# Optimization experiments

Measured on AMD Instinct MI355X. Metric: run time of the kernel, lower is better.

## Reference

```python
import jax, jax.numpy as jnp
import numpy as np

N = 50000
E = 500000
D = 128
L = 3
BN_EPS = 1e-5


def setup_inputs() -> dict:
    key = jax.random.key(0)
    ks = jax.random.split(key, 16)

    def xavier(k, shape):
        fan_in, fan_out = shape[-2], shape[-1]
        limit = float(np.sqrt(6.0 / (fan_in + fan_out)))
        return jax.random.uniform(k, shape, jnp.float32, -limit, limit)

    inp = {
        "x": jax.random.randint(ks[0], (N, 2), 0, 3),
        "edge_index": jax.random.randint(ks[1], (2, E), 0, N),
        "edge_attr": jax.random.randint(ks[2], (E, 2), 0, 3),
        # atom embeddings (xavier_uniform like torch init)
        "atom_emb0": xavier(ks[3], (120, D)),
        "atom_emb1": xavier(ks[4], (3, D)),
        # per-layer edge embeddings, stacked over layers
        "edge_emb0": xavier(ks[5], (L, 5, D)),
        "edge_emb1": xavier(ks[6], (L, 3, D)),
        # per-layer MLP: Linear(D, 2D) -> ReLU -> Linear(2D, D)
        "W1": xavier(ks[7], (L, D, 2 * D)),
        "b1": jnp.zeros((L, 2 * D), jnp.float32),
        "W2": xavier(ks[8], (L, 2 * D, D)),
        "b2": jnp.zeros((L, D), jnp.float32),
        # batchnorm affine params
        "gamma": jnp.ones((L, D), jnp.float32),
        "beta": jnp.zeros((L, D), jnp.float32),
    }
    return inp


def reference(x, edge_index, edge_attr, atom_emb0, atom_emb1,
              edge_emb0, edge_emb1, W1, b1, W2, b2, gamma, beta):
    n = x.shape[0]
    num_layer = W1.shape[0]

    # atom embedding: sum of per-attribute embeddings -> [N, D]
    h = atom_emb0[x[:, 0]] + atom_emb1[x[:, 1]]

    # add self loops: src/dst both get arange(N) appended
    loop = jnp.arange(n, dtype=edge_index.dtype)
    src = jnp.concatenate([edge_index[0], loop])  # [E+N]
    dst = jnp.concatenate([edge_index[1], loop])  # [E+N]
    # self-loop edge attr is [4, 0]
    ea0 = jnp.concatenate([edge_attr[:, 0], jnp.full((n,), 4, edge_attr.dtype)])
    ea1 = jnp.concatenate([edge_attr[:, 1], jnp.zeros((n,), edge_attr.dtype)])

    for l in range(num_layer):
        # edge embedding lookup + message = x_j + edge_attr, scatter-add to dst
        eemb = edge_emb0[l][ea0] + edge_emb1[l][ea1]          # [E+N, D]
        msg = h[src] + eemb                                   # gather + add
        aggr = jax.ops.segment_sum(msg, dst, num_segments=n)  # [N, D]
        # MLP update
        hid = jax.nn.relu(aggr @ W1[l] + b1[l])               # [N, 2D]
        out = hid @ W2[l] + b2[l]                             # [N, D]
        # BatchNorm1d (training mode: batch stats, biased variance)
        mean = jnp.mean(out, axis=0)
        var = jnp.mean(jnp.square(out - mean), axis=0)
        out = gamma[l] * (out - mean) * jax.lax.rsqrt(var + BN_EPS) + beta[l]
        # dropout with p=0 is identity; ReLU on all but last layer
        h = out if l == num_layer - 1 else jax.nn.relu(out)
    return h
```

## Files before the change

### kernel.cpp

```cpp
#include <hip/hip_runtime.h>

#define D 128
#define TWO_D 256
#define BN_EPS 1e-5f

typedef __attribute__((ext_vector_type(8))) short bf16x8;
typedef __attribute__((ext_vector_type(4))) float f32x4;

__device__ __forceinline__ float relu_f(float x) { return x > 0.f ? x : 0.f; }

__device__ __forceinline__ unsigned short f2bf(float f) {
    unsigned u = __builtin_bit_cast(unsigned, f);
    return (unsigned short)((u + 0x7FFFu + ((u >> 16) & 1u)) >> 16);
}
__device__ __forceinline__ float bf2f(unsigned s) {
    unsigned u = s << 16;
    return __builtin_bit_cast(float, u);
}
__device__ __forceinline__ unsigned pack2(float a, float b) {
    return (unsigned)f2bf(a) | ((unsigned)f2bf(b) << 16);
}

__global__ void atom_embed_kernel(const int* __restrict__ x,
                                  const float* __restrict__ emb0,
                                  const float* __restrict__ emb1,
                                  unsigned short* __restrict__ hbf, int n) {
    int idx = blockIdx.x * blockDim.x + threadIdx.x;
    if (idx >= n * 32) return;
    int node = idx >> 5;
    int d0 = (idx & 31) << 2;
    int i0 = x[node * 2 + 0];
    int i1 = x[node * 2 + 1];
    const float4 a = *reinterpret_cast<const float4*>(emb0 + (size_t)i0 * D + d0);
    const float4 b = *reinterpret_cast<const float4*>(emb1 + (size_t)i1 * D + d0);
    uint2 v;
    v.x = pack2(a.x + b.x, a.y + b.y);
    v.y = pack2(a.z + b.z, a.w + b.w);
    *reinterpret_cast<uint2*>(hbf + (size_t)node * D + d0) = v;
}

__global__ void hist_kernel(const int* __restrict__ ei, int* __restrict__ counts, int e_cnt) {
    int e = blockIdx.x * blockDim.x + threadIdx.x;
    if (e >= e_cnt) return;
    atomicAdd(counts + ei[e_cnt + e], 1);
}

__global__ __launch_bounds__(256) void bsum_kernel(const int* __restrict__ counts,
                                                   int* __restrict__ bsum, int n) {
    __shared__ int s[256];
    int t = threadIdx.x;
    int idx = blockIdx.x * 256 + t;
    s[t] = (idx < n) ? counts[idx] : 0;
    __syncthreads();
    for (int off = 128; off > 0; off >>= 1) {
        if (t < off) s[t] += s[t + off];
        __syncthreads();
    }
    if (t == 0) bsum[blockIdx.x] = s[0];
}

__global__ __launch_bounds__(256) void bscan_kernel(const int* __restrict__ bsum,
                                                    int* __restrict__ bpre,
                                                    int* __restrict__ row_ptr, int nb, int n) {
    __shared__ int s[256];
    int t = threadIdx.x;
    s[t] = (t < nb) ? bsum[t] : 0;
    __syncthreads();
    for (int off = 1; off < 256; off <<= 1) {
        int v = (t >= off) ? s[t - off] : 0;
        __syncthreads();
        s[t] += v;
        __syncthreads();
    }
    bpre[t] = (t == 0) ? 0 : s[t - 1];
    if (t == 255) row_ptr[n] = s[255];
}

__global__ __launch_bounds__(256) void scan_apply_kernel(const int* __restrict__ counts,
                                                         const int* __restrict__ bpre,
                                                         int* __restrict__ row_ptr,
                                                         int* __restrict__ cursor, int n) {
    __shared__ int s[256];
    int t = threadIdx.x;
    int idx = blockIdx.x * 256 + t;
    int c = (idx < n) ? counts[idx] : 0;
    s[t] = c;
    __syncthreads();
    for (int off = 1; off < 256; off <<= 1) {
        int v = (t >= off) ? s[t - off] : 0;
        __syncthreads();
        s[t] += v;
        __syncthreads();
    }
    if (idx < n) {
        int excl = bpre[blockIdx.x] + s[t] - c;
        row_ptr[idx] = excl;
        cursor[idx] = excl;
    }
}

__global__ void fill_kernel(const int* __restrict__ ei, const int* __restrict__ ea,
                            int* __restrict__ cursor, int* __restrict__ epack, int e_cnt) {
    int e = blockIdx.x * blockDim.x + threadIdx.x;
    if (e >= e_cnt) return;
    int dst = ei[e_cnt + e];
    int src = ei[e];
    int aidx = ea[e * 2 + 0] * 3 + ea[e * 2 + 1];
    int pos = atomicAdd(cursor + dst, 1);
    epack[pos] = (src & 0x1FFFF) | (aidx << 17);
}

__global__ void frag_prep_kernel(const float* __restrict__ W1,
                                 const float* __restrict__ W2,
                                 unsigned short* __restrict__ w1f,
                                 unsigned short* __restrict__ w2f, int Lnum) {
    int tid = blockIdx.x * blockDim.x + threadIdx.x;
    if (tid >= Lnum * 128 * 64) return;
    int l = tid / 8192;
    int rem = tid % 8192;
    int frag = rem / 64;
    int lane = rem % 64;
    int kg = lane >> 4, cl = lane & 15;
    if (frag < 64) {
        int kk = frag >> 4, tn = frag & 15;
        const float* src = W1 + (size_t)l * D * TWO_D;
        int k0 = kk * 32 + kg * 8, col = tn * 16 + cl;
        unsigned short* dst = w1f + (size_t)l * 32768 + ((size_t)frag * 64 + lane) * 8;
        #pragma unroll
        for (int j = 0; j < 8; ++j) dst[j] = f2bf(src[(size_t)(k0 + j) * TWO_D + col]);
    } else {
        int f2 = frag - 64;
        int kk = f2 >> 3, tn = f2 & 7;
        const float* src = W2 + (size_t)l * TWO_D * D;
        int k0 = kk * 32 + kg * 8, col = tn * 16 + cl;
        unsigned short* dst = w2f + (size_t)l * 32768 + ((size_t)f2 * 64 + lane) * 8;
        #pragma unroll
        for (int j = 0; j < 8; ++j) dst[j] = f2bf(src[(size_t)(k0 + j) * D + col]);
    }
}

template<int DO_BN>
__global__ __launch_bounds__(256) void gather_kernel(
    const unsigned short* __restrict__ hbf,
    const float* __restrict__ ee0_l, const float* __restrict__ ee1_l,
    const float* __restrict__ stats_prev,
    const float* __restrict__ gamma_p, const float* __restrict__ beta_p,
    float inv_n,
    const int* __restrict__ row_ptr, const int* __restrict__ epack,
    unsigned short* __restrict__ aggrbf, float* __restrict__ stats_cur, int n) {

    __shared__ float cee[16 * D];
    __shared__ float sbn[2 * D];
    const int t = threadIdx.x;
    if (blockIdx.x == 0) stats_cur[t] = 0.f;
    for (int i = t; i < 16 * D; i += 256) {
        int r = i >> 7, d = i & 127;
        cee[i] = (r < 15) ? ee0_l[(r / 3) * D + d] + ee1_l[(r % 3) * D + d]
                          : ee0_l[4 * D + d] + ee1_l[d];
    }
    if (DO_BN && t < 128) {
        float mean = stats_prev[t] * inv_n;
        float var  = stats_prev[128 + t] * inv_n - mean * mean;
        float sc = gamma_p[t] * rsqrtf(var + BN_EPS);
        sbn[t] = sc;
        sbn[128 + t] = beta_p[t] - mean * sc;
    }
    __syncthreads();

    int node = blockIdx.x * 8 + (t >> 5);
    if (node >= n) return;
    int d0 = (t & 31) << 2;

    float4 sc = make_float4(1.f, 1.f, 1.f, 1.f);
    float4 sh = make_float4(0.f, 0.f, 0.f, 0.f);
    if (DO_BN) {
        sc = *reinterpret_cast<const float4*>(sbn + d0);
        sh = *reinterpret_cast<const float4*>(sbn + 128 + d0);
    }

    const int jb = row_ptr[node];
    const int je = row_ptr[node + 1];

    float ax, ay, az, aw;
    {
        const float4 cs = *reinterpret_cast<const float4*>(cee + 15 * D + d0);
        uint2 hv = *reinterpret_cast<const uint2*>(hbf + (size_t)node * D + d0);
        if (DO_BN) {
            ax = relu_f(bf2f(hv.x & 0xffffu) * sc.x + sh.x) + cs.x;
            ay = relu_f(bf2f(hv.x >> 16)     * sc.y + sh.y) + cs.y;
            az = relu_f(bf2f(hv.y & 0xffffu) * sc.z + sh.z) + cs.z;
            aw = relu_f(bf2f(hv.y >> 16)     * sc.w + sh.w) + cs.w;
        } else {
            ax = bf2f(hv.x & 0xffffu) + cs.x;
            ay = bf2f(hv.x >> 16)     + cs.y;
            az = bf2f(hv.y & 0xffffu) + cs.z;
            aw = bf2f(hv.y >> 16)     + cs.w;
        }
    }

    unsigned long long c0 = 0ull;
    int cnt8 = 0;

#define ROWLD(p) (*reinterpret_cast<const uint2*>(hbf + (size_t)((p) & 0x1FFFF) * D + d0))
#define CNTUPD(p) do { int a_ = (p) >> 17; \
        unsigned long long bit_ = 1ull << ((a_ & 7) << 3); \
        c0 += (a_ < 8) ? bit_ : 0ull; cnt8 += (a_ >> 3); } while (0)
#define EACC(sv) do { \
        if (DO_BN) { \
            ax += relu_f(bf2f((sv).x & 0xffffu) * sc.x + sh.x); \
            ay += relu_f(bf2f((sv).x >> 16)     * sc.y + sh.y); \
            az += relu_f(bf2f((sv).y & 0xffffu) * sc.z + sh.z); \
            aw += relu_f(bf2f((sv).y >> 16)     * sc.w + sh.w); \
        } else { \
            ax += bf2f((sv).x & 0xffffu); ay += bf2f((sv).x >> 16); \
            az += bf2f((sv).y & 0xffffu); aw += bf2f((sv).y >> 16); \
        } } while (0)

    int j = jb;
    for (; j + 8 <= je; j += 8) {
        const int p0 = epack[j + 0], p1 = epack[j + 1], p2 = epack[j + 2], p3 = epack[j + 3];
        const int p4 = epack[j + 4], p5 = epack[j + 5], p6 = epack[j + 6], p7 = epack[j + 7];
        const uint2 s0 = ROWLD(p0), s1 = ROWLD(p1), s2 = ROWLD(p2), s3 = ROWLD(p3);
        const uint2 s4 = ROWLD(p4), s5 = ROWLD(p5), s6 = ROWLD(p6), s7 = ROWLD(p7);
        CNTUPD(p0); CNTUPD(p1); CNTUPD(p2); CNTUPD(p3);
        CNTUPD(p4); CNTUPD(p5); CNTUPD(p6); CNTUPD(p7);
        EACC(s0); EACC(s1); EACC(s2); EACC(s3);
        EACC(s4); EACC(s5); EACC(s6); EACC(s7);
    }
    for (; j < je; ++j) {
        const int p = epack[j];
        const uint2 sv = ROWLD(p);
        CNTUPD(p);
        EACC(sv);
    }

    #pragma unroll
    for (int a = 0; a < 8; ++a) {
        float fc = (float)((unsigned)(c0 >> (a * 8)) & 0xFFu);
        const float4 ev = *reinterpret_cast<const float4*>(cee + a * D + d0);
        ax += fc * ev.x; ay += fc * ev.y; az += fc * ev.z; aw += fc * ev.w;
    }
    {
        float fc = (float)cnt8;
        const float4 ev = *reinterpret_cast<const float4*>(cee + 8 * D + d0);
        ax += fc * ev.x; ay += fc * ev.y; az += fc * ev.z; aw += fc * ev.w;
    }

    uint2 o;
    o.x = pack2(ax, ay);
    o.y = pack2(az, aw);
    *reinterpret_cast<uint2*>(aggrbf + (size_t)node * D + d0) = o;
#undef ROWLD
#undef CNTUPD
#undef EACC
}

__global__ __launch_bounds__(256) void mlp_mfma_kernel(
    unsigned short* __restrict__ aggrbf,
    const bf16x8* __restrict__ w1f, const bf16x8* __restrict__ w2f,
    const float* __restrict__ b1l, const float* __restrict__ b2l,
    float* __restrict__ outf, float* __restrict__ stats, int n, int final_f32) {

    __shared__ unsigned short hid[32 * TWO_D];
    __shared__ float sred[256];

    const int wave = threadIdx.x >> 6;
    const int lane = threadIdx.x & 63;
    const int arow = lane & 15;
    const int kgrp = lane >> 4;

    bf16x8 W1[4][4];
    #pragma unroll
    for (int kk = 0; kk < 4; ++kk)
        #pragma unroll
        for (int t = 0; t < 4; ++t)
            W1[kk][t] = w1f[(kk * 16 + wave * 4 + t) * 64 + lane];
    bf16x8 W2[8][2];
    #pragma unroll
    for (int kk = 0; kk < 8; ++kk)
        #pragma unroll
        for (int t = 0; t < 2; ++t)
            W2[kk][t] = w2f[(kk * 8 + wave * 2 + t) * 64 + lane];

    float b1v[4], b2v[2];
    #pragma unroll
    for (int t = 0; t < 4; ++t) b1v[t] = b1l[wave * 64 + t * 16 + arow];
    #pragma unroll
    for (int t = 0; t < 2; ++t) b2v[t] = b2l[wave * 32 + t * 16 + arow];

    float ps[2] = {0.f, 0.f}, pq[2] = {0.f, 0.f};

    const int tiles = n >> 4;
    const int npair = (tiles + 1) >> 1;
    for (int p = blockIdx.x; p < npair; p += gridDim.x) {
        const int t0i = 2 * p, t1i = 2 * p + 1;
        const bool has1 = (t1i < tiles);
        const size_t r0 = (size_t)t0i * 16, r1 = (size_t)t1i * 16;

        bf16x8 a0[4], a1[4];
        #pragma unroll
        for (int kk = 0; kk < 4; ++kk)
            a0[kk] = *reinterpret_cast<const bf16x8*>(
                aggrbf + (r0 + arow) * D + kk * 32 + kgrp * 8);
        if (has1) {
            #pragma unroll
            for (int kk = 0; kk < 4; ++kk)
                a1[kk] = *reinterpret_cast<const bf16x8*>(
                    aggrbf + (r1 + arow) * D + kk * 32 + kgrp * 8);
        }

        f32x4 acc1[4];
        #pragma unroll
        for (int t = 0; t < 4; ++t) acc1[t] = (f32x4){0.f, 0.f, 0.f, 0.f};
        #pragma unroll
        for (int kk = 0; kk < 4; ++kk)
            #pragma unroll
            for (int t = 0; t < 4; ++t)
                acc1[t] = __builtin_amdgcn_mfma_f32_16x16x32_bf16(a0[kk], W1[kk][t], acc1[t], 0, 0, 0);

        __syncthreads();
        #pragma unroll
        for (int t = 0; t < 4; ++t) {
            const int cc = wave * 64 + t * 16 + arow;
            #pragma unroll
            for (int r = 0; r < 4; ++r) {
                const int rr = kgrp * 4 + r;
                hid[(rr * TWO_D + cc) ^ ((rr & 7) << 3)] = f2bf(relu_f(acc1[t][r] + b1v[t]));
            }
        }

        if (has1) {
            #pragma unroll
            for (int t = 0; t < 4; ++t) acc1[t] = (f32x4){0.f, 0.f, 0.f, 0.f};
            #pragma unroll
            for (int kk = 0; kk < 4; ++kk)
                #pragma unroll
                for (int t = 0; t < 4; ++t)
                    acc1[t] = __builtin_amdgcn_mfma_f32_16x16x32_bf16(a1[kk], W1[kk][t], acc1[t], 0, 0, 0);
            #pragma unroll
            for (int t = 0; t < 4; ++t) {
                const int cc = wave * 64 + t * 16 + arow;
                #pragma unroll
                for (int r = 0; r < 4; ++r) {
                    const int rr = 16 + kgrp * 4 + r;
                    hid[(rr * TWO_D + cc) ^ ((rr & 7) << 3)] = f2bf(relu_f(acc1[t][r] + b1v[t]));
                }
            }
        }
        __syncthreads();

        {
            f32x4 acc2[2];
            #pragma unroll
            for (int t = 0; t < 2; ++t) acc2[t] = (f32x4){0.f, 0.f, 0.f, 0.f};
            #pragma unroll
            for (int kk = 0; kk < 8; ++kk) {
                bf16x8 a2 = *reinterpret_cast<const bf16x8*>(
                    hid + ((arow * TWO_D + kk * 32 + kgrp * 8) ^ ((arow & 7) << 3)));
                #pragma unroll
                for (int t = 0; t < 2; ++t)
                    acc2[t] = __builtin_amdgcn_mfma_f32_16x16x32_bf16(a2, W2[kk][t], acc2[t], 0, 0, 0);
            }
            #pragma unroll
            for (int t = 0; t < 2; ++t) {
                const int col = wave * 32 + t * 16 + arow;
                #pragma unroll
                for (int r = 0; r < 4; ++r) {
                    float v = acc2[t][r] + b2v[t];
                    if (final_f32) outf[(r0 + kgrp * 4 + r) * D + col] = v;
                    else           aggrbf[(r0 + kgrp * 4 + r) * D + col] = f2bf(v);
                    ps[t] += v; pq[t] += v * v;
                }
            }
        }
        if (has1) {
            f32x4 acc2[2];
            #pragma unroll
            for (int t = 0; t < 2; ++t) acc2[t] = (f32x4){0.f, 0.f, 0.f, 0.f};
            #pragma unroll
            for (int kk = 0; kk < 8; ++kk) {
                bf16x8 a2 = *reinterpret_cast<const bf16x8*>(
                    hid + (((16 + arow) * TWO_D + kk * 32 + kgrp * 8) ^ ((arow & 7) << 3)));
                #pragma unroll
                for (int t = 0; t < 2; ++t)
                    acc2[t] = __builtin_amdgcn_mfma_f32_16x16x32_bf16(a2, W2[kk][t], acc2[t], 0, 0, 0);
            }
            #pragma unroll
            for (int t = 0; t < 2; ++t) {
                const int col = wave * 32 + t * 16 + arow;
                #pragma unroll
                for (int r = 0; r < 4; ++r) {
                    float v = acc2[t][r] + b2v[t];
                    if (final_f32) outf[(r1 + kgrp * 4 + r) * D + col] = v;
                    else           aggrbf[(r1 + kgrp * 4 + r) * D + col] = f2bf(v);
                    ps[t] += v; pq[t] += v * v;
                }
            }
        }
    }

    sred[threadIdx.x] = 0.f;
    __syncthreads();
    #pragma unroll
    for (int t = 0; t < 2; ++t) {
        const int col = wave * 32 + t * 16 + arow;
        atomicAdd(sred + col, ps[t]);
        atomicAdd(sred + 128 + col, pq[t]);
    }
    __syncthreads();
    unsafeAtomicAdd(stats + threadIdx.x, sred[threadIdx.x]);
}

__global__ void bn_apply_final_kernel(const float* __restrict__ out,
                                      const float* __restrict__ stats,
                                      const float* __restrict__ gamma_l,
                                      const float* __restrict__ beta_l,
                                      float inv_n,
                                      float* __restrict__ dst, int n) {
    __shared__ float sbn[2 * D];
    int t = threadIdx.x;
    if (t < 128) {
        float mean = stats[t] * inv_n;
        float var  = stats[128 + t] * inv_n - mean * mean;
        float sc = gamma_l[t] * rsqrtf(var + BN_EPS);
        sbn[t] = sc;
        sbn[128 + t] = beta_l[t] - mean * sc;
    }
    __syncthreads();
    int idx = blockIdx.x * blockDim.x + t;
    if (idx >= n * 32) return;
    int d0 = (idx & 31) << 2;
    float4 v  = *reinterpret_cast<const float4*>(out + (size_t)idx * 4);
    float4 sc = *reinterpret_cast<const float4*>(sbn + d0);
    float4 sh = *reinterpret_cast<const float4*>(sbn + 128 + d0);
    *reinterpret_cast<float4*>(dst + (size_t)idx * 4) =
        make_float4(v.x * sc.x + sh.x, v.y * sc.y + sh.y,
                    v.z * sc.z + sh.z, v.w * sc.w + sh.w);
}

extern "C" void kernel_launch(void* const* d_in, const int* in_sizes, int n_in,
                              void* d_out, int out_size, void* d_ws, size_t ws_size,
                              hipStream_t stream) {
    const int*   x     = (const int*)d_in[0];
    const int*   ei    = (const int*)d_in[1];
    const int*   ea    = (const int*)d_in[2];
    const float* aemb0 = (const float*)d_in[3];
    const float* aemb1 = (const float*)d_in[4];
    const float* eemb0 = (const float*)d_in[5];
    const float* eemb1 = (const float*)d_in[6];
    const float* W1    = (const float*)d_in[7];
    const float* b1    = (const float*)d_in[8];
    const float* W2    = (const float*)d_in[9];
    const float* b2    = (const float*)d_in[10];
    const float* gamma = (const float*)d_in[11];
    const float* beta  = (const float*)d_in[12];

    const int n = in_sizes[0] / 2;
    const int e = in_sizes[1] / 2;
    const int L = in_sizes[8] / TWO_D;
    const float inv_n = 1.0f / (float)n;

    char* ws = (char*)d_ws;
    float* outb = (float*)ws;                      ws += (size_t)n * D * 4;
    unsigned short* bufA = (unsigned short*)ws;    ws += (size_t)n * D * 2;
    unsigned short* bufB = (unsigned short*)ws;    ws += (size_t)n * D * 2;
    unsigned short* w1f = (unsigned short*)ws;     ws += (size_t)L * 32768 * 2;
    unsigned short* w2f = (unsigned short*)ws;     ws += (size_t)L * 32768 * 2;
    float* statsA = (float*)ws;                    ws += 256 * 4;
    float* statsB = (float*)ws;                    ws += 256 * 4;
    int* counts  = (int*)ws;                       ws += (size_t)n * 4;
    int* row_ptr = (int*)ws;                       ws += (size_t)(n + 1) * 4;
    int* cursor  = (int*)ws;                       ws += (size_t)n * 4;
    int* bsum    = (int*)ws;                       ws += 256 * 4;
    int* bpre    = (int*)ws;                       ws += 256 * 4;
    int* epack   = (int*)ws;

    const int edge_blocks = (e + 255) / 256;
    const int vec_blocks  = (n * 32 + 255) / 256;
    const int node_blocks = (n + 7) / 8;
    const int nb = (n + 255) / 256;

    hipMemsetAsync(counts, 0, (size_t)n * sizeof(int), stream);
    hist_kernel<<<edge_blocks, 256, 0, stream>>>(ei, counts, e);
    bsum_kernel<<<nb, 256, 0, stream>>>(counts, bsum, n);
    bscan_kernel<<<1, 256, 0, stream>>>(bsum, bpre, row_ptr, nb, n);
    scan_apply_kernel<<<nb, 256, 0, stream>>>(counts, bpre, row_ptr, cursor, n);
    fill_kernel<<<edge_blocks, 256, 0, stream>>>(ei, ea, cursor, epack, e);
    frag_prep_kernel<<<(L * 128 * 64 + 255) / 256, 256, 0, stream>>>(W1, W2, w1f, w2f, L);
    atom_embed_kernel<<<vec_blocks, 256, 0, stream>>>(x, aemb0, aemb1, bufA, n);

    for (int l = 0; l < L; ++l) {
        const float* ee0_l = eemb0 + (size_t)l * 5 * D;
        const float* ee1_l = eemb1 + (size_t)l * 3 * D;
        const float* b1l   = b1 + (size_t)l * TWO_D;
        const float* b2l   = b2 + (size_t)l * D;

        unsigned short* src = (l & 1) ? bufB : bufA;
        unsigned short* dst = (l & 1) ? bufA : bufB;
        float* stats_cur  = (l & 1) ? statsB : statsA;
        float* stats_prev = (l & 1) ? statsA : statsB;

        if (l == 0)
            gather_kernel<0><<<node_blocks, 256, 0, stream>>>(
                src, ee0_l, ee1_l, nullptr, nullptr, nullptr, inv_n,
                row_ptr, epack, dst, stats_cur, n);
        else
            gather_kernel<1><<<node_blocks, 256, 0, stream>>>(
                src, ee0_l, ee1_l, stats_prev,
                gamma + (size_t)(l - 1) * D, beta + (size_t)(l - 1) * D, inv_n,
                row_ptr, epack, dst, stats_cur, n);

        mlp_mfma_kernel<<<512, 256, 0, stream>>>(
            dst,
            (const bf16x8*)(w1f + (size_t)l * 32768),
            (const bf16x8*)(w2f + (size_t)l * 32768),
            b1l, b2l, outb, stats_cur, n, (l == L - 1) ? 1 : 0);
    }

    float* stats_last = ((L - 1) & 1) ? statsB : statsA;
    bn_apply_final_kernel<<<vec_blocks, 256, 0, stream>>>(
        outb, stats_last, gamma + (size_t)(L - 1) * D, beta + (size_t)(L - 1) * D,
        inv_n, (float*)d_out, n);
}
```

Baseline: 278.8 us.

## Pad CSR rows to multiples of 8 with 16-bit source ids and separate BN pass

The CSR build now pads each row to a multiple of eight entries, filling the padding with a zero node row, and stores source indices as 16-bit values. Edge-attribute counts are computed once per node in the histogram kernel rather than decoded per edge on every layer. The gather kernel loads eight indices at a time with one vector load and uses no tail loop. BatchNorm plus ReLU moves out of the gather's per-edge path into a separate bn_mid kernel that writes bf16 once per layer, which adds a full pass over an fp32 buffer each layer. The 16-bit indices rely on N fitting in 16 bits, and the padding adds gather reads of the zero row.

```diff
diff --git a/kernel.cpp b/kernel.cpp
--- a/kernel.cpp
+++ b/kernel.cpp
@@ -25,6 +25,8 @@
                                   const float* __restrict__ emb0,
                                   const float* __restrict__ emb1,
                                   unsigned short* __restrict__ hbf, int n) {
+    if (blockIdx.x == 0 && threadIdx.x < 64)
+        reinterpret_cast<unsigned*>(hbf + (size_t)n * D)[threadIdx.x] = 0u;
     int idx = blockIdx.x * blockDim.x + threadIdx.x;
     if (idx >= n * 32) return;
     int node = idx >> 5;
@@ -39,18 +41,25 @@
     *reinterpret_cast<uint2*>(hbf + (size_t)node * D + d0) = v;
 }
 
-__global__ void hist_kernel(const int* __restrict__ ei, int* __restrict__ counts, int e_cnt) {
+__global__ void hist_kernel(const int* __restrict__ ei, const int* __restrict__ ea,
+                            int* __restrict__ counts,
+                            unsigned long long* __restrict__ cnts, int e_cnt) {
     int e = blockIdx.x * blockDim.x + threadIdx.x;
     if (e >= e_cnt) return;
-    atomicAdd(counts + ei[e_cnt + e], 1);
-}
+    int dst = ei[e_cnt + e];
+    atomicAdd(counts + dst, 1);
+    int aidx = ea[e * 2 + 0] * 3 + ea[e * 2 + 1];
+    if (aidx < 8) atomicAdd(cnts + dst, 1ull << (aidx * 8));
+}
+
+__device__ __forceinline__ int pad8(int d) { return (d + 7) & ~7; }
 
 __global__ __launch_bounds__(256) void bsum_kernel(const int* __restrict__ counts,
                                                    int* __restrict__ bsum, int n) {
     __shared__ int s[256];
     int t = threadIdx.x;
     int idx = blockIdx.x * 256 + t;
-    s[t] = (idx < n) ? counts[idx] : 0;
+    s[t] = (idx < n) ? pad8(counts[idx]) : 0;
     __syncthreads();
     for (int off = 128; off > 0; off >>= 1) {
         if (t < off) s[t] += s[t + off];
@@ -61,7 +70,7 @@
 
 __global__ __launch_bounds__(256) void bscan_kernel(const int* __restrict__ bsum,
                                                     int* __restrict__ bpre,
-                                                    int* __restrict__ row_ptr, int nb, int n) {
+                                                    int* __restrict__ rpp, int nb, int n) {
     __shared__ int s[256];
     int t = threadIdx.x;
     s[t] = (t < nb) ? bsum[t] : 0;
@@ -73,17 +82,17 @@
         __syncthreads();
     }
     bpre[t] = (t == 0) ? 0 : s[t - 1];
-    if (t == 255) row_ptr[n] = s[255];
+    if (t == 255) rpp[n] = s[255];
 }
 
 __global__ __launch_bounds__(256) void scan_apply_kernel(const int* __restrict__ counts,
                                                          const int* __restrict__ bpre,
-                                                         int* __restrict__ row_ptr,
+                                                         int* __restrict__ rpp,
                                                          int* __restrict__ cursor, int n) {
     __shared__ int s[256];
     int t = threadIdx.x;
     int idx = blockIdx.x * 256 + t;
-    int c = (idx < n) ? counts[idx] : 0;
+    int c = (idx < n) ? pad8(counts[idx]) : 0;
     s[t] = c;
     __syncthreads();
     for (int off = 1; off < 256; off <<= 1) {
@@ -94,20 +103,31 @@
     }
     if (idx < n) {
         int excl = bpre[blockIdx.x] + s[t] - c;
-        row_ptr[idx] = excl;
+        rpp[idx] = excl;
         cursor[idx] = excl;
     }
 }
 
-__global__ void fill_kernel(const int* __restrict__ ei, const int* __restrict__ ea,
-                            int* __restrict__ cursor, int* __restrict__ epack, int e_cnt) {
+__global__ void fill_kernel(const int* __restrict__ ei,
+                            int* __restrict__ cursor,
+                            unsigned short* __restrict__ ep, int e_cnt) {
     int e = blockIdx.x * blockDim.x + threadIdx.x;
     if (e >= e_cnt) return;
     int dst = ei[e_cnt + e];
     int src = ei[e];
-    int aidx = ea[e * 2 + 0] * 3 + ea[e * 2 + 1];
     int pos = atomicAdd(cursor + dst, 1);
-    epack[pos] = (src & 0x1FFFF) | (aidx << 17);
+    ep[pos] = (unsigned short)src;
+}
+
+__global__ void pad_kernel(const int* __restrict__ cursor, const int* __restrict__ counts,
+                           const int* __restrict__ rpp,
+                           unsigned short* __restrict__ ep, int n) {
+    int i = blockIdx.x * blockDim.x + threadIdx.x;
+    if (i >= n) return;
+    int b = cursor[i];
+    int e = rpp[i] + pad8(counts[i]);
+    unsigned short zr = (unsigned short)n;
+    for (int j = b; j < e; ++j) ep[j] = zr;
 }
 
 __global__ void frag_prep_kernel(const float* __restrict__ W1,
@@ -139,127 +159,94 @@
     }
 }
 
-template<int DO_BN>
 __global__ __launch_bounds__(256) void gather_kernel(
     const unsigned short* __restrict__ hbf,
     const float* __restrict__ ee0_l, const float* __restrict__ ee1_l,
-    const float* __restrict__ stats_prev,
-    const float* __restrict__ gamma_p, const float* __restrict__ beta_p,
-    float inv_n,
-    const int* __restrict__ row_ptr, const int* __restrict__ epack,
-    unsigned short* __restrict__ aggrbf, float* __restrict__ stats_cur, int n) {
+    const int* __restrict__ rpp, const int* __restrict__ counts,
+    const unsigned long long* __restrict__ cnts,
+    const unsigned short* __restrict__ ep,
+    unsigned short* __restrict__ aggrbf, float* __restrict__ stats, int n) {
 
     __shared__ float cee[16 * D];
-    __shared__ float sbn[2 * D];
     const int t = threadIdx.x;
-    if (blockIdx.x == 0) stats_cur[t] = 0.f;
+    if (blockIdx.x == 0) stats[t] = 0.f;
     for (int i = t; i < 16 * D; i += 256) {
         int r = i >> 7, d = i & 127;
         cee[i] = (r < 15) ? ee0_l[(r / 3) * D + d] + ee1_l[(r % 3) * D + d]
                           : ee0_l[4 * D + d] + ee1_l[d];
     }
-    if (DO_BN && t < 128) {
-        float mean = stats_prev[t] * inv_n;
-        float var  = stats_prev[128 + t] * inv_n - mean * mean;
-        float sc = gamma_p[t] * rsqrtf(var + BN_EPS);
-        sbn[t] = sc;
-        sbn[128 + t] = beta_p[t] - mean * sc;
-    }
     __syncthreads();
 
     int node = blockIdx.x * 8 + (t >> 5);
     if (node >= n) return;
     int d0 = (t & 31) << 2;
 
-    float4 sc = make_float4(1.f, 1.f, 1.f, 1.f);
-    float4 sh = make_float4(0.f, 0.f, 0.f, 0.f);
-    if (DO_BN) {
-        sc = *reinterpret_cast<const float4*>(sbn + d0);
-        sh = *reinterpret_cast<const float4*>(sbn + 128 + d0);
-    }
-
-    const int jb = row_ptr[node];
-    const int je = row_ptr[node + 1];
+    const int jb = rpp[node];
+    const int deg = counts[node];
+    const unsigned long long c0 = cnts[node];
+    const int nch = pad8(deg) >> 3;
 
     float ax, ay, az, aw;
     {
         const float4 cs = *reinterpret_cast<const float4*>(cee + 15 * D + d0);
         uint2 hv = *reinterpret_cast<const uint2*>(hbf + (size_t)node * D + d0);
-        if (DO_BN) {
-            ax = relu_f(bf2f(hv.x & 0xffffu) * sc.x + sh.x) + cs.x;
-            ay = relu_f(bf2f(hv.x >> 16)     * sc.y + sh.y) + cs.y;
-            az = relu_f(bf2f(hv.y & 0xffffu) * sc.z + sh.z) + cs.z;
-            aw = relu_f(bf2f(hv.y >> 16)     * sc.w + sh.w) + cs.w;
-        } else {
-            ax = bf2f(hv.x & 0xffffu) + cs.x;
-            ay = bf2f(hv.x >> 16)     + cs.y;
-            az = bf2f(hv.y & 0xffffu) + cs.z;
-            aw = bf2f(hv.y >> 16)     + cs.w;
-        }
-    }
-
-    unsigned long long c0 = 0ull;
-    int cnt8 = 0;
-
-#define ROWLD(p) (*reinterpret_cast<const uint2*>(hbf + (size_t)((p) & 0x1FFFF) * D + d0))
-#define CNTUPD(p) do { int a_ = (p) >> 17; \
-        unsigned long long bit_ = 1ull << ((a_ & 7) << 3); \
-        c0 += (a_ < 8) ? bit_ : 0ull; cnt8 += (a_ >> 3); } while (0)
-#define EACC(sv) do { \
-        if (DO_BN) { \
-            ax += relu_f(bf2f((sv).x & 0xffffu) * sc.x + sh.x); \
-            ay += relu_f(bf2f((sv).x >> 16)     * sc.y + sh.y); \
-            az += relu_f(bf2f((sv).y & 0xffffu) * sc.z + sh.z); \
-            aw += relu_f(bf2f((sv).y >> 16)     * sc.w + sh.w); \
-        } else { \
-            ax += bf2f((sv).x & 0xffffu); ay += bf2f((sv).x >> 16); \
-            az += bf2f((sv).y & 0xffffu); aw += bf2f((sv).y >> 16); \
-        } } while (0)
-
-    int j = jb;
-    for (; j + 8 <= je; j += 8) {
-        const int p0 = epack[j + 0], p1 = epack[j + 1], p2 = epack[j + 2], p3 = epack[j + 3];
-        const int p4 = epack[j + 4], p5 = epack[j + 5], p6 = epack[j + 6], p7 = epack[j + 7];
-        const uint2 s0 = ROWLD(p0), s1 = ROWLD(p1), s2 = ROWLD(p2), s3 = ROWLD(p3);
-        const uint2 s4 = ROWLD(p4), s5 = ROWLD(p5), s6 = ROWLD(p6), s7 = ROWLD(p7);
-        CNTUPD(p0); CNTUPD(p1); CNTUPD(p2); CNTUPD(p3);
-        CNTUPD(p4); CNTUPD(p5); CNTUPD(p6); CNTUPD(p7);
-        EACC(s0); EACC(s1); EACC(s2); EACC(s3);
-        EACC(s4); EACC(s5); EACC(s6); EACC(s7);
-    }
-    for (; j < je; ++j) {
-        const int p = epack[j];
-        const uint2 sv = ROWLD(p);
-        CNTUPD(p);
-        EACC(sv);
-    }
-
+        ax = bf2f(hv.x & 0xffffu) + cs.x;
+        ay = bf2f(hv.x >> 16)     + cs.y;
+        az = bf2f(hv.y & 0xffffu) + cs.z;
+        aw = bf2f(hv.y >> 16)     + cs.w;
+    }
+
+    int csum = 0;
     #pragma unroll
     for (int a = 0; a < 8; ++a) {
-        float fc = (float)((unsigned)(c0 >> (a * 8)) & 0xFFu);
+        int fc = (int)((c0 >> (a * 8)) & 0xFFull);
+        csum += fc;
+        float f = (float)fc;
         const float4 ev = *reinterpret_cast<const float4*>(cee + a * D + d0);
-        ax += fc * ev.x; ay += fc * ev.y; az += fc * ev.z; aw += fc * ev.w;
+        ax += f * ev.x; ay += f * ev.y; az += f * ev.z; aw += f * ev.w;
     }
     {
-        float fc = (float)cnt8;
+        float f = (float)(deg - csum);
         const float4 ev = *reinterpret_cast<const float4*>(cee + 8 * D + d0);
-        ax += fc * ev.x; ay += fc * ev.y; az += fc * ev.z; aw += fc * ev.w;
-    }
+        ax += f * ev.x; ay += f * ev.y; az += f * ev.z; aw += f * ev.w;
+    }
+
+#define ROWLD(s) (*reinterpret_cast<const uint2*>(hbf + (size_t)(s) * D + d0))
+#define EACC(sv) do { \
+        ax += bf2f((sv).x & 0xffffu); ay += bf2f((sv).x >> 16); \
+        az += bf2f((sv).y & 0xffffu); aw += bf2f((sv).y >> 16); } while (0)
+#define PROC(iv) do { \
+        const uint2 s0 = ROWLD((iv).x & 0xFFFFu), s1 = ROWLD((iv).x >> 16); \
+        const uint2 s2 = ROWLD((iv).y & 0xFFFFu), s3 = ROWLD((iv).y >> 16); \
+        const uint2 s4 = ROWLD((iv).z & 0xFFFFu), s5 = ROWLD((iv).z >> 16); \
+        const uint2 s6 = ROWLD((iv).w & 0xFFFFu), s7 = ROWLD((iv).w >> 16); \
+        EACC(s0); EACC(s1); EACC(s2); EACC(s3); \
+        EACC(s4); EACC(s5); EACC(s6); EACC(s7); } while (0)
+
+    if (nch) {
+        uint4 iv = *reinterpret_cast<const uint4*>(ep + jb);
+        for (int c = 1; c < nch; ++c) {
+            uint4 nx = *reinterpret_cast<const uint4*>(ep + jb + 8 * c);
+            PROC(iv);
+            iv = nx;
+        }
+        PROC(iv);
+    }
+#undef ROWLD
+#undef EACC
+#undef PROC
 
     uint2 o;
     o.x = pack2(ax, ay);
     o.y = pack2(az, aw);
     *reinterpret_cast<uint2*>(aggrbf + (size_t)node * D + d0) = o;
-#undef ROWLD
-#undef CNTUPD
-#undef EACC
 }
 
 __global__ __launch_bounds__(256) void mlp_mfma_kernel(
-    unsigned short* __restrict__ aggrbf,
+    const unsigned short* __restrict__ aggrbf,
     const bf16x8* __restrict__ w1f, const bf16x8* __restrict__ w2f,
     const float* __restrict__ b1l, const float* __restrict__ b2l,
-    float* __restrict__ outf, float* __restrict__ stats, int n, int final_f32) {
+    float* __restrict__ outf, float* __restrict__ stats, int n) {
 
     __shared__ unsigned short hid[32 * TWO_D];
     __shared__ float sred[256];
@@ -328,7 +315,6 @@
                 hid[(rr * TWO_D + cc) ^ ((rr & 7) << 3)] = f2bf(relu_f(acc1[t][r] + b1v[t]));
             }
         }
-
         if (has1) {
             #pragma unroll
             for (int t = 0; t < 4; ++t) acc1[t] = (f32x4){0.f, 0.f, 0.f, 0.f};
@@ -367,8 +353,7 @@
                 #pragma unroll
                 for (int r = 0; r < 4; ++r) {
                     float v = acc2[t][r] + b2v[t];
-                    if (final_f32) outf[(r0 + kgrp * 4 + r) * D + col] = v;
-                    else           aggrbf[(r0 + kgrp * 4 + r) * D + col] = f2bf(v);
+                    outf[(r0 + kgrp * 4 + r) * D + col] = v;
                     ps[t] += v; pq[t] += v * v;
                 }
             }
@@ -391,8 +376,7 @@
                 #pragma unroll
                 for (int r = 0; r < 4; ++r) {
                     float v = acc2[t][r] + b2v[t];
-                    if (final_f32) outf[(r1 + kgrp * 4 + r) * D + col] = v;
-                    else           aggrbf[(r1 + kgrp * 4 + r) * D + col] = f2bf(v);
+                    outf[(r1 + kgrp * 4 + r) * D + col] = v;
                     ps[t] += v; pq[t] += v * v;
                 }
             }
@@ -409,6 +393,36 @@
     }
     __syncthreads();
     unsafeAtomicAdd(stats + threadIdx.x, sred[threadIdx.x]);
+}
+
+__global__ void bn_mid_kernel(const float* __restrict__ out,
+                              const float* __restrict__ stats,
+                              const float* __restrict__ gamma_l,
+                              const float* __restrict__ beta_l,
+                              float inv_n,
+                              unsigned short* __restrict__ dsth, int n) {
+    __shared__ float sbn[2 * D];
+    int t = threadIdx.x;
+    if (blockIdx.x == 0 && t >= 128 && t < 192)
+        reinterpret_cast<unsigned*>(dsth + (size_t)n * D)[t - 128] = 0u;
+    if (t < 128) {
+        float mean = stats[t] * inv_n;
+        float var  = stats[128 + t] * inv_n - mean * mean;
+        float sc = gamma_l[t] * rsqrtf(var + BN_EPS);
+        sbn[t] = sc;
+        sbn[128 + t] = beta_l[t] - mean * sc;
+    }
+    __syncthreads();
+    int idx = blockIdx.x * blockDim.x + t;
+    if (idx >= n * 32) return;
+    int d0 = (idx & 31) << 2;
+    float4 v  = *reinterpret_cast<const float4*>(out + (size_t)idx * 4);
+    float4 sc = *reinterpret_cast<const float4*>(sbn + d0);
+    float4 sh = *reinterpret_cast<const float4*>(sbn + 128 + d0);
+    uint2 o;
+    o.x = pack2(relu_f(v.x * sc.x + sh.x), relu_f(v.y * sc.y + sh.y));
+    o.y = pack2(relu_f(v.z * sc.z + sh.z), relu_f(v.w * sc.w + sh.w));
+    *reinterpret_cast<uint2*>(dsth + (size_t)idx * 4) = o;
 }
 
 __global__ void bn_apply_final_kernel(const float* __restrict__ out,
@@ -462,63 +476,58 @@
 
     char* ws = (char*)d_ws;
     float* outb = (float*)ws;                      ws += (size_t)n * D * 4;
-    unsigned short* bufA = (unsigned short*)ws;    ws += (size_t)n * D * 2;
-    unsigned short* bufB = (unsigned short*)ws;    ws += (size_t)n * D * 2;
+    unsigned short* buf0 = (unsigned short*)ws;    ws += (size_t)(n + 1) * D * 2;
+    unsigned short* buf1 = (unsigned short*)ws;    ws += (size_t)(n + 1) * D * 2;
+    unsigned short* bufC = (unsigned short*)ws;    ws += (size_t)n * D * 2;
     unsigned short* w1f = (unsigned short*)ws;     ws += (size_t)L * 32768 * 2;
     unsigned short* w2f = (unsigned short*)ws;     ws += (size_t)L * 32768 * 2;
-    float* statsA = (float*)ws;                    ws += 256 * 4;
-    float* statsB = (float*)ws;                    ws += 256 * 4;
+    float* stats = (float*)ws;                     ws += 256 * 4;
     int* counts  = (int*)ws;                       ws += (size_t)n * 4;
-    int* row_ptr = (int*)ws;                       ws += (size_t)(n + 1) * 4;
+    unsigned long long* cnts = (unsigned long long*)ws;  ws += (size_t)n * 8;
+    int* rpp     = (int*)ws;                       ws += (size_t)(n + 4) * 4;
     int* cursor  = (int*)ws;                       ws += (size_t)n * 4;
     int* bsum    = (int*)ws;                       ws += 256 * 4;
     int* bpre    = (int*)ws;                       ws += 256 * 4;
-    int* epack   = (int*)ws;
+    unsigned short* epack = (unsigned short*)ws;
 
     const int edge_blocks = (e + 255) / 256;
     const int vec_blocks  = (n * 32 + 255) / 256;
     const int node_blocks = (n + 7) / 8;
     const int nb = (n + 255) / 256;
 
-    hipMemsetAsync(counts, 0, (size_t)n * sizeof(int), stream);
-    hist_kernel<<<edge_blocks, 256, 0, stream>>>(ei, counts, e);
+    hipMemsetAsync(counts, 0, (size_t)n * 4 + (size_t)n * 8, stream);
+    hist_kernel<<<edge_blocks, 256, 0, stream>>>(ei, ea, counts, cnts, e);
     bsum_kernel<<<nb, 256, 0, stream>>>(counts, bsum, n);
-    bscan_kernel<<<1, 256, 0, stream>>>(bsum, bpre, row_ptr, nb, n);
-    scan_apply_kernel<<<nb, 256, 0, stream>>>(counts, bpre, row_ptr, cursor, n);
-    fill_kernel<<<edge_blocks, 256, 0, stream>>>(ei, ea, cursor, epack, e);
+    bscan_kernel<<<1, 256, 0, stream>>>(bsum, bpre, rpp, nb, n);
+    scan_apply_kernel<<<nb, 256, 0, stream>>>(counts, bpre, rpp, cursor, n);
+    fill_kernel<<<edge_blocks, 256, 0, stream>>>(ei, cursor, epack, e);
+    pad_kernel<<<nb, 256, 0, stream>>>(cursor, counts, rpp, epack, n);
     frag_prep_kernel<<<(L * 128 * 64 + 255) / 256, 256, 0, stream>>>(W1, W2, w1f, w2f, L);
-    atom_embed_kernel<<<vec_blocks, 256, 0, stream>>>(x, aemb0, aemb1, bufA, n);
+    atom_embed_kernel<<<vec_blocks, 256, 0, stream>>>(x, aemb0, aemb1, buf0, n);
 
     for (int l = 0; l < L; ++l) {
         const float* ee0_l = eemb0 + (size_t)l * 5 * D;
         const float* ee1_l = eemb1 + (size_t)l * 3 * D;
-        const float* b1l   = b1 + (size_t)l * TWO_D;
-        const float* b2l   = b2 + (size_t)l * D;
-
-        unsigned short* src = (l & 1) ? bufB : bufA;
-        unsigned short* dst = (l & 1) ? bufA : bufB;
-        float* stats_cur  = (l & 1) ? statsB : statsA;
-        float* stats_prev = (l & 1) ? statsA : statsB;
-
-        if (l == 0)
-            gather_kernel<0><<<node_blocks, 256, 0, stream>>>(
-                src, ee0_l, ee1_l, nullptr, nullptr, nullptr, inv_n,
-                row_ptr, epack, dst, stats_cur, n);
-        else
-            gather_kernel<1><<<node_blocks, 256, 0, stream>>>(
-                src, ee0_l, ee1_l, stats_prev,
-                gamma + (size_t)(l - 1) * D, beta + (size_t)(l - 1) * D, inv_n,
-                row_ptr, epack, dst, stats_cur, n);
-
+
+        unsigned short* hsrc = (l & 1) ? buf1 : buf0;
+
+        gather_kernel<<<node_blocks, 256, 0, stream>>>(
+            hsrc, ee0_l, ee1_l, rpp, counts, cnts, epack, bufC, stats, n);
         mlp_mfma_kernel<<<512, 256, 0, stream>>>(
-            dst,
+            bufC,
             (const bf16x8*)(w1f + (size_t)l * 32768),
             (const bf16x8*)(w2f + (size_t)l * 32768),
-            b1l, b2l, outb, stats_cur, n, (l == L - 1) ? 1 : 0);
-    }
-
-    float* stats_last = ((L - 1) & 1) ? statsB : statsA;
-    bn_apply_final_kernel<<<vec_blocks, 256, 0, stream>>>(
-        outb, stats_last, gamma + (size_t)(L - 1) * D, beta + (size_t)(L - 1) * D,
-        inv_n, (float*)d_out, n);
-}
+            b1 + (size_t)l * TWO_D, b2 + (size_t)l * D, outb, stats, n);
+
+        if (l < L - 1) {
+            unsigned short* hdst = (l & 1) ? buf0 : buf1;
+            bn_mid_kernel<<<vec_blocks, 256, 0, stream>>>(
+                outb, stats, gamma + (size_t)l * D, beta + (size_t)l * D,
+                inv_n, hdst, n);
+        } else {
+            bn_apply_final_kernel<<<vec_blocks, 256, 0, stream>>>(
+                outb, stats, gamma + (size_t)l * D, beta + (size_t)l * D,
+                inv_n, (float*)d_out, n);
+        }
+    }
+}
```

Measured after the change: 301.0 us. +8.0%, slower.

## Pad CSR rows to 8 with 16-bit source indices and precomputed attr counts

Applied to the files above, without the earlier changes.

Rebuilds the CSR so each node's edge list is padded to a multiple of 8 and stores source indices as 16-bit values in a new conversion pass. That pass also precomputes per-node edge-attribute counts. The gather kernel then loads 8 indices with a single 128-bit load, prefetches the next chunk, and skips per-edge attribute decoding. Padding slots point at a zero row appended to each feature buffer, and under batchnorm the ReLU of the shift is subtracted for them. Risk: 16-bit indices cannot address N=50000 plus the zero row beyond 65535, so this depends on N staying small; it also adds a setup kernel and extra workspace.

```diff
diff --git a/kernel.cpp b/kernel.cpp
--- a/kernel.cpp
+++ b/kernel.cpp
@@ -21,10 +21,17 @@
     return (unsigned)f2bf(a) | ((unsigned)f2bf(b) << 16);
 }
 
+__device__ __forceinline__ int pad8(int d) { return (d + 7) & ~7; }
+
 __global__ void atom_embed_kernel(const int* __restrict__ x,
                                   const float* __restrict__ emb0,
                                   const float* __restrict__ emb1,
-                                  unsigned short* __restrict__ hbf, int n) {
+                                  unsigned short* __restrict__ bufA,
+                                  unsigned short* __restrict__ bufB, int n) {
+    if (blockIdx.x == 0 && threadIdx.x < 64)
+        reinterpret_cast<unsigned*>(bufA + (size_t)n * D)[threadIdx.x] = 0u;
+    if (blockIdx.x == 1 && threadIdx.x < 64)
+        reinterpret_cast<unsigned*>(bufB + (size_t)n * D)[threadIdx.x] = 0u;
     int idx = blockIdx.x * blockDim.x + threadIdx.x;
     if (idx >= n * 32) return;
     int node = idx >> 5;
@@ -36,7 +43,7 @@
     uint2 v;
     v.x = pack2(a.x + b.x, a.y + b.y);
     v.y = pack2(a.z + b.z, a.w + b.w);
-    *reinterpret_cast<uint2*>(hbf + (size_t)node * D + d0) = v;
+    *reinterpret_cast<uint2*>(bufA + (size_t)node * D + d0) = v;
 }
 
 __global__ void hist_kernel(const int* __restrict__ ei, int* __restrict__ counts, int e_cnt) {
@@ -50,7 +57,7 @@
     __shared__ int s[256];
     int t = threadIdx.x;
     int idx = blockIdx.x * 256 + t;
-    s[t] = (idx < n) ? counts[idx] : 0;
+    s[t] = (idx < n) ? pad8(counts[idx]) : 0;
     __syncthreads();
     for (int off = 128; off > 0; off >>= 1) {
         if (t < off) s[t] += s[t + off];
@@ -61,7 +68,7 @@
 
 __global__ __launch_bounds__(256) void bscan_kernel(const int* __restrict__ bsum,
                                                     int* __restrict__ bpre,
-                                                    int* __restrict__ row_ptr, int nb, int n) {
+                                                    int* __restrict__ rpp, int nb, int n) {
     __shared__ int s[256];
     int t = threadIdx.x;
     s[t] = (t < nb) ? bsum[t] : 0;
@@ -73,17 +80,17 @@
         __syncthreads();
     }
     bpre[t] = (t == 0) ? 0 : s[t - 1];
-    if (t == 255) row_ptr[n] = s[255];
+    if (t == 255) rpp[n] = s[255];
 }
 
 __global__ __launch_bounds__(256) void scan_apply_kernel(const int* __restrict__ counts,
                                                          const int* __restrict__ bpre,
-                                                         int* __restrict__ row_ptr,
+                                                         int* __restrict__ rpp,
                                                          int* __restrict__ cursor, int n) {
     __shared__ int s[256];
     int t = threadIdx.x;
     int idx = blockIdx.x * 256 + t;
-    int c = (idx < n) ? counts[idx] : 0;
+    int c = (idx < n) ? pad8(counts[idx]) : 0;
     s[t] = c;
     __syncthreads();
     for (int off = 1; off < 256; off <<= 1) {
@@ -94,20 +101,42 @@
     }
     if (idx < n) {
         int excl = bpre[blockIdx.x] + s[t] - c;
-        row_ptr[idx] = excl;
+        rpp[idx] = excl;
         cursor[idx] = excl;
     }
 }
 
 __global__ void fill_kernel(const int* __restrict__ ei, const int* __restrict__ ea,
-                            int* __restrict__ cursor, int* __restrict__ epack, int e_cnt) {
+                            int* __restrict__ cursor,
+                            unsigned* __restrict__ ep32, int e_cnt) {
     int e = blockIdx.x * blockDim.x + threadIdx.x;
     if (e >= e_cnt) return;
     int dst = ei[e_cnt + e];
     int src = ei[e];
     int aidx = ea[e * 2 + 0] * 3 + ea[e * 2 + 1];
     int pos = atomicAdd(cursor + dst, 1);
-    epack[pos] = (src & 0x1FFFF) | (aidx << 17);
+    ep32[pos] = (unsigned)(src & 0x1FFFF) | ((unsigned)aidx << 17);
+}
+
+__global__ void convert_kernel(const int* __restrict__ rpp, const int* __restrict__ counts,
+                               const unsigned* __restrict__ ep32,
+                               unsigned short* __restrict__ ep16,
+                               unsigned long long* __restrict__ cnts, int n) {
+    int i = blockIdx.x * blockDim.x + threadIdx.x;
+    if (i >= n) return;
+    const int jb = rpp[i];
+    const int deg = counts[i];
+    const int pe = pad8(deg);
+    unsigned long long c = 0ull;
+    int j = 0;
+    for (; j < deg; ++j) {
+        unsigned v = ep32[jb + j];
+        ep16[jb + j] = (unsigned short)(v & 0xFFFFu);
+        int a = (int)(v >> 17);
+        if (a < 8) c += 1ull << (a * 8);
+    }
+    for (; j < pe; ++j) ep16[jb + j] = (unsigned short)n;
+    cnts[i] = c;
 }
 
 __global__ void frag_prep_kernel(const float* __restrict__ W1,
@@ -146,7 +175,9 @@
     const float* __restrict__ stats_prev,
     const float* __restrict__ gamma_p, const float* __restrict__ beta_p,
     float inv_n,
-    const int* __restrict__ row_ptr, const int* __restrict__ epack,
+    const int* __restrict__ rpp, const int* __restrict__ counts,
+    const unsigned long long* __restrict__ cnts,
+    const unsigned short* __restrict__ ep,
     unsigned short* __restrict__ aggrbf, float* __restrict__ stats_cur, int n) {
 
     __shared__ float cee[16 * D];
@@ -173,13 +204,17 @@
 
     float4 sc = make_float4(1.f, 1.f, 1.f, 1.f);
     float4 sh = make_float4(0.f, 0.f, 0.f, 0.f);
+    float4 rsh = make_float4(0.f, 0.f, 0.f, 0.f);
     if (DO_BN) {
         sc = *reinterpret_cast<const float4*>(sbn + d0);
         sh = *reinterpret_cast<const float4*>(sbn + 128 + d0);
-    }
-
-    const int jb = row_ptr[node];
-    const int je = row_ptr[node + 1];
+        rsh = make_float4(relu_f(sh.x), relu_f(sh.y), relu_f(sh.z), relu_f(sh.w));
+    }
+
+    const int jb = rpp[node];
+    const int deg = counts[node];
+    const unsigned long long c0 = cnts[node];
+    const int nch = pad8(deg) >> 3;
 
     float ax, ay, az, aw;
     {
@@ -198,13 +233,22 @@
         }
     }
 
-    unsigned long long c0 = 0ull;
-    int cnt8 = 0;
-
-#define ROWLD(p) (*reinterpret_cast<const uint2*>(hbf + (size_t)((p) & 0x1FFFF) * D + d0))
-#define CNTUPD(p) do { int a_ = (p) >> 17; \
-        unsigned long long bit_ = 1ull << ((a_ & 7) << 3); \
-        c0 += (a_ < 8) ? bit_ : 0ull; cnt8 += (a_ >> 3); } while (0)
+    int csum = 0;
+    #pragma unroll
+    for (int a = 0; a < 8; ++a) {
+        int fc = (int)((c0 >> (a * 8)) & 0xFFull);
+        csum += fc;
+        float f = (float)fc;
+        const float4 ev = *reinterpret_cast<const float4*>(cee + a * D + d0);
+        ax += f * ev.x; ay += f * ev.y; az += f * ev.z; aw += f * ev.w;
+    }
+    {
+        float f = (float)(deg - csum);
+        const float4 ev = *reinterpret_cast<const float4*>(cee + 8 * D + d0);
+        ax += f * ev.x; ay += f * ev.y; az += f * ev.z; aw += f * ev.w;
+    }
+
+#define ROWLD(s_) (*reinterpret_cast<const uint2*>(hbf + (size_t)(s_) * D + d0))
 #define EACC(sv) do { \
         if (DO_BN) { \
             ax += relu_f(bf2f((sv).x & 0xffffu) * sc.x + sh.x); \
@@ -215,44 +259,36 @@
             ax += bf2f((sv).x & 0xffffu); ay += bf2f((sv).x >> 16); \
             az += bf2f((sv).y & 0xffffu); aw += bf2f((sv).y >> 16); \
         } } while (0)
-
-    int j = jb;
-    for (; j + 8 <= je; j += 8) {
-        const int p0 = epack[j + 0], p1 = epack[j + 1], p2 = epack[j + 2], p3 = epack[j + 3];
-        const int p4 = epack[j + 4], p5 = epack[j + 5], p6 = epack[j + 6], p7 = epack[j + 7];
-        const uint2 s0 = ROWLD(p0), s1 = ROWLD(p1), s2 = ROWLD(p2), s3 = ROWLD(p3);
-        const uint2 s4 = ROWLD(p4), s5 = ROWLD(p5), s6 = ROWLD(p6), s7 = ROWLD(p7);
-        CNTUPD(p0); CNTUPD(p1); CNTUPD(p2); CNTUPD(p3);
-        CNTUPD(p4); CNTUPD(p5); CNTUPD(p6); CNTUPD(p7);
-        EACC(s0); EACC(s1); EACC(s2); EACC(s3);
-        EACC(s4); EACC(s5); EACC(s6); EACC(s7);
-    }
-    for (; j < je; ++j) {
-        const int p = epack[j];
-        const uint2 sv = ROWLD(p);
-        CNTUPD(p);
-        EACC(sv);
-    }
-
-    #pragma unroll
-    for (int a = 0; a < 8; ++a) {
-        float fc = (float)((unsigned)(c0 >> (a * 8)) & 0xFFu);
-        const float4 ev = *reinterpret_cast<const float4*>(cee + a * D + d0);
-        ax += fc * ev.x; ay += fc * ev.y; az += fc * ev.z; aw += fc * ev.w;
-    }
-    {
-        float fc = (float)cnt8;
-        const float4 ev = *reinterpret_cast<const float4*>(cee + 8 * D + d0);
-        ax += fc * ev.x; ay += fc * ev.y; az += fc * ev.z; aw += fc * ev.w;
+#define PROC(iv) do { \
+        const uint2 s0 = ROWLD((iv).x & 0xFFFFu), s1 = ROWLD((iv).x >> 16); \
+        const uint2 s2 = ROWLD((iv).y & 0xFFFFu), s3 = ROWLD((iv).y >> 16); \
+        const uint2 s4 = ROWLD((iv).z & 0xFFFFu), s5 = ROWLD((iv).z >> 16); \
+        const uint2 s6 = ROWLD((iv).w & 0xFFFFu), s7 = ROWLD((iv).w >> 16); \
+        EACC(s0); EACC(s1); EACC(s2); EACC(s3); \
+        EACC(s4); EACC(s5); EACC(s6); EACC(s7); } while (0)
+
+    if (nch) {
+        uint4 iv = *reinterpret_cast<const uint4*>(ep + jb);
+        for (int c = 1; c < nch; ++c) {
+            uint4 nx = *reinterpret_cast<const uint4*>(ep + jb + 8 * c);
+            PROC(iv);
+            iv = nx;
+        }
+        PROC(iv);
+    }
+#undef ROWLD
+#undef EACC
+#undef PROC
+
+    if (DO_BN) {
+        float np = (float)(pad8(deg) - deg);
+        ax -= np * rsh.x; ay -= np * rsh.y; az -= np * rsh.z; aw -= np * rsh.w;
     }
 
     uint2 o;
     o.x = pack2(ax, ay);
     o.y = pack2(az, aw);
     *reinterpret_cast<uint2*>(aggrbf + (size_t)node * D + d0) = o;
-#undef ROWLD
-#undef CNTUPD
-#undef EACC
 }
 
 __global__ __launch_bounds__(256) void mlp_mfma_kernel(
@@ -328,7 +364,6 @@
                 hid[(rr * TWO_D + cc) ^ ((rr & 7) << 3)] = f2bf(relu_f(acc1[t][r] + b1v[t]));
             }
         }
-
         if (has1) {
             #pragma unroll
             for (int t = 0; t < 4; ++t) acc1[t] = (f32x4){0.f, 0.f, 0.f, 0.f};
@@ -462,38 +497,39 @@
 
     char* ws = (char*)d_ws;
     float* outb = (float*)ws;                      ws += (size_t)n * D * 4;
-    unsigned short* bufA = (unsigned short*)ws;    ws += (size_t)n * D * 2;
-    unsigned short* bufB = (unsigned short*)ws;    ws += (size_t)n * D * 2;
+    unsigned short* bufA = (unsigned short*)ws;    ws += (size_t)(n + 1) * D * 2;
+    unsigned short* bufB = (unsigned short*)ws;    ws += (size_t)(n + 1) * D * 2;
     unsigned short* w1f = (unsigned short*)ws;     ws += (size_t)L * 32768 * 2;
     unsigned short* w2f = (unsigned short*)ws;     ws += (size_t)L * 32768 * 2;
     float* statsA = (float*)ws;                    ws += 256 * 4;
     float* statsB = (float*)ws;                    ws += 256 * 4;
     int* counts  = (int*)ws;                       ws += (size_t)n * 4;
-    int* row_ptr = (int*)ws;                       ws += (size_t)(n + 1) * 4;
+    unsigned long long* cnts = (unsigned long long*)ws;  ws += (size_t)n * 8;
+    int* rpp     = (int*)ws;                       ws += (size_t)(n + 4) * 4;
     int* cursor  = (int*)ws;                       ws += (size_t)n * 4;
     int* bsum    = (int*)ws;                       ws += 256 * 4;
     int* bpre    = (int*)ws;                       ws += 256 * 4;
-    int* epack   = (int*)ws;
+    unsigned* ep32 = (unsigned*)ws;                ws += ((size_t)e + 8 * (size_t)n) * 4;
+    unsigned short* ep16 = (unsigned short*)ws;
 
     const int edge_blocks = (e + 255) / 256;
     const int vec_blocks  = (n * 32 + 255) / 256;
     const int node_blocks = (n + 7) / 8;
     const int nb = (n + 255) / 256;
 
-    hipMemsetAsync(counts, 0, (size_t)n * sizeof(int), stream);
+    hipMemsetAsync(counts, 0, (size_t)n * 4, stream);
     hist_kernel<<<edge_blocks, 256, 0, stream>>>(ei, counts, e);
     bsum_kernel<<<nb, 256, 0, stream>>>(counts, bsum, n);
-    bscan_kernel<<<1, 256, 0, stream>>>(bsum, bpre, row_ptr, nb, n);
-    scan_apply_kernel<<<nb, 256, 0, stream>>>(counts, bpre, row_ptr, cursor, n);
-    fill_kernel<<<edge_blocks, 256, 0, stream>>>(ei, ea, cursor, epack, e);
+    bscan_kernel<<<1, 256, 0, stream>>>(bsum, bpre, rpp, nb, n);
+    scan_apply_kernel<<<nb, 256, 0, stream>>>(counts, bpre, rpp, cursor, n);
+    fill_kernel<<<edge_blocks, 256, 0, stream>>>(ei, ea, cursor, ep32, e);
+    convert_kernel<<<nb, 256, 0, stream>>>(rpp, counts, ep32, ep16, cnts, n);
     frag_prep_kernel<<<(L * 128 * 64 + 255) / 256, 256, 0, stream>>>(W1, W2, w1f, w2f, L);
-    atom_embed_kernel<<<vec_blocks, 256, 0, stream>>>(x, aemb0, aemb1, bufA, n);
+    atom_embed_kernel<<<vec_blocks, 256, 0, stream>>>(x, aemb0, aemb1, bufA, bufB, n);
 
     for (int l = 0; l < L; ++l) {
         const float* ee0_l = eemb0 + (size_t)l * 5 * D;
         const float* ee1_l = eemb1 + (size_t)l * 3 * D;
-        const float* b1l   = b1 + (size_t)l * TWO_D;
-        const float* b2l   = b2 + (size_t)l * D;
 
         unsigned short* src = (l & 1) ? bufB : bufA;
         unsigned short* dst = (l & 1) ? bufA : bufB;
@@ -503,18 +539,19 @@
         if (l == 0)
             gather_kernel<0><<<node_blocks, 256, 0, stream>>>(
                 src, ee0_l, ee1_l, nullptr, nullptr, nullptr, inv_n,
-                row_ptr, epack, dst, stats_cur, n);
+                rpp, counts, cnts, ep16, dst, stats_cur, n);
         else
             gather_kernel<1><<<node_blocks, 256, 0, stream>>>(
                 src, ee0_l, ee1_l, stats_prev,
                 gamma + (size_t)(l - 1) * D, beta + (size_t)(l - 1) * D, inv_n,
-                row_ptr, epack, dst, stats_cur, n);
+                rpp, counts, cnts, ep16, dst, stats_cur, n);
 
         mlp_mfma_kernel<<<512, 256, 0, stream>>>(
             dst,
             (const bf16x8*)(w1f + (size_t)l * 32768),
             (const bf16x8*)(w2f + (size_t)l * 32768),
-            b1l, b2l, outb, stats_cur, n, (l == L - 1) ? 1 : 0);
+            b1 + (size_t)l * TWO_D, b2 + (size_t)l * D,
+            outb, stats_cur, n, (l == L - 1) ? 1 : 0);
     }
 
     float* stats_last = ((L - 1) & 1) ? statsB : statsA;
```

Measured after the change: 268.3 us. 3.8% less time.
